# Kernel tuning notes

Measured on AMD Instinct MI355X. Metric: run time of the kernel, lower is better.

Reference implementation:

```python
import math
import jax, jax.numpy as jnp
import numpy as np

B, T, E = 2, 2048, 1024
H, KV = 16, 4
D = E // H          # 64
G = H // KV         # 4 groups


def rotate_half(x):
    x1, x2 = jnp.split(x, 2, axis=-1)
    return jnp.concatenate([-x2, x1], axis=-1)


def setup_inputs() -> dict:
    key = jax.random.key(0)
    ks = jax.random.split(key, 12)
    query = jax.random.normal(ks[0], (B, T, E), jnp.float32)
    key_t = jax.random.normal(ks[1], (B, T, E), jnp.float32)
    value = jax.random.normal(ks[2], (B, T, E), jnp.float32)
    # RoPE tables: [T, D]
    inv_freq = 1.0 / (10000.0 ** (np.arange(0, D, 2, dtype=np.float32) / D))
    pos = np.arange(T, dtype=np.float32)
    freqs = np.outer(pos, inv_freq)                      # [T, D/2]
    emb = np.concatenate([freqs, freqs], axis=-1)        # [T, D]
    cos_emb = jnp.asarray(np.cos(emb), jnp.float32)
    sin_emb = jnp.asarray(np.sin(emb), jnp.float32)
    # causal mask [1,1,T,T], True = keep
    mask = jnp.tril(jnp.ones((T, T), bool))[None, None, :, :]
    s = 0.02
    Wq = jax.random.normal(ks[3], (E, H * D), jnp.float32) * s
    bq = jnp.zeros((H * D,), jnp.float32)
    Wk = jax.random.normal(ks[4], (E, KV * D), jnp.float32) * s
    bk = jnp.zeros((KV * D,), jnp.float32)
    Wv = jax.random.normal(ks[5], (E, KV * D), jnp.float32) * s
    bv = jnp.zeros((KV * D,), jnp.float32)
    Wo = jax.random.normal(ks[6], (E, E), jnp.float32) * s
    bo = jnp.zeros((E,), jnp.float32)
    return {"query": query, "key": key_t, "value": value,
            "cos_emb": cos_emb, "sin_emb": sin_emb, "mask": mask,
            "Wq": Wq, "bq": bq, "Wk": Wk, "bk": bk,
            "Wv": Wv, "bv": bv, "Wo": Wo, "bo": bo}


def reference(query, key, value, cos_emb, sin_emb, mask,
              Wq, bq, Wk, bk, Wv, bv, Wo, bo):
    Bq, Tq, _ = query.shape
    Tk = key.shape[1]
    q = (query @ Wq + bq).reshape(Bq, Tq, H, D)          # [B,Tq,H,D]
    k = (key @ Wk + bk).reshape(Bq, Tk, KV, D)           # [B,Tk,KV,D]
    v = (value @ Wv + bv).reshape(Bq, Tk, KV, D)
    # expand kv heads across groups (head h = kv*G + g, consecutive repeat)
    k = jnp.repeat(k, G, axis=2)                         # [B,Tk,H,D]
    v = jnp.repeat(v, G, axis=2)
    # RoPE (applied post-expansion, as in the original)
    cos = cos_emb[None, :, None, :]                      # [1,T,1,D]
    sin = sin_emb[None, :, None, :]
    q = q * cos[:, :Tq] + rotate_half(q) * sin[:, :Tq]
    k = k * cos[:, :Tk] + rotate_half(k) * sin[:, :Tk]
    scores = jnp.einsum('bqhd,bkhd->bhqk', q, k) / math.sqrt(D)
    scores = jnp.where(mask[:, :, :Tq, :Tk], scores, jnp.float32(-jnp.inf))
    probs = jax.nn.softmax(scores, axis=-1)              # [B,H,Tq,Tk]
    attn = jnp.einsum('bhqk,bkhd->bqhd', probs, v).reshape(Bq, Tq, E)
    return attn @ Wo + bo
```

## Files before the change

### kernel.cpp

```cpp
#include <hip/hip_runtime.h>
#include <hip/hip_bf16.h>

constexpr int Bc  = 2;
constexpr int Tc  = 2048;
constexpr int Ec  = 1024;
constexpr int Hc  = 16;
constexpr int KVc = 4;
constexpr int Dc  = 64;

typedef short bf16x8 __attribute__((ext_vector_type(8)));
typedef short short4v __attribute__((ext_vector_type(4)));
typedef float f32x4  __attribute__((ext_vector_type(4)));
typedef float f32x16 __attribute__((ext_vector_type(16)));
typedef int   i32x4  __attribute__((ext_vector_type(4)));

__device__ inline short f2bf_bits(float f) {
    union { __hip_bfloat16 h; short s; } u;
    u.h = __float2bfloat16(f);
    return u.s;
}

__device__ inline float bf2f(short s) {
    union { short s16; __hip_bfloat16 h; } u;
    u.s16 = s;
    return __bfloat162float(u.h);
}

__device__ inline unsigned pkbf(float a, float b) {
    return (unsigned)(unsigned short)f2bf_bits(a)
         | ((unsigned)(unsigned short)f2bf_bits(b) << 16);
}

__device__ inline float fexp2(float x) { return __builtin_exp2f(x); }

__device__ inline void gload16(const short* g, short* lds) {
    __builtin_amdgcn_global_load_lds(
        (const __attribute__((address_space(1))) unsigned int*)g,
        (__attribute__((address_space(3))) unsigned int*)lds,
        16, 0, 0);
}

__global__ __launch_bounds__(256) void conv3_f32_bf16(
    const float* __restrict__ q, const float* __restrict__ k,
    const float* __restrict__ v,
    short* __restrict__ Xq, short* __restrict__ Xk, short* __restrict__ Xv)
{
    const int range = blockIdx.x >> 12;
    const int sub   = blockIdx.x & 4095;
    const float* x = range == 0 ? q : (range == 1 ? k : v);
    short*       y = range == 0 ? Xq : (range == 1 ? Xk : Xv);
    int i = (sub * 256 + threadIdx.x) * 4;
    float4 vv = *reinterpret_cast<const float4*>(x + i);
    short4v o;
    o[0] = f2bf_bits(vv.x);
    o[1] = f2bf_bits(vv.y);
    o[2] = f2bf_bits(vv.z);
    o[3] = f2bf_bits(vv.w);
    *reinterpret_cast<short4v*>(y + i) = o;
}

__global__ __launch_bounds__(256) void transp_all(
    const float* __restrict__ Wq, const float* __restrict__ Wk,
    const float* __restrict__ Wv, const float* __restrict__ Wo,
    short* __restrict__ Wqt, short* __restrict__ Wkt,
    short* __restrict__ Wvt, short* __restrict__ Wot)
{
    __shared__ float tile[32][33];
    const int id = blockIdx.x;
    const float* W; short* Wt; int N, bx, by;
    if (id < 1024)      { W = Wq; Wt = Wqt; N = 1024; bx = id & 31;          by = id >> 5; }
    else if (id < 1280) { W = Wk; Wt = Wkt; N = 256;  bx = (id - 1024) & 7;  by = (id - 1024) >> 3; }
    else if (id < 1536) { W = Wv; Wt = Wvt; N = 256;  bx = (id - 1280) & 7;  by = (id - 1280) >> 3; }
    else                { W = Wo; Wt = Wot; N = 1024; bx = (id - 1536) & 31; by = (id - 1536) >> 5; }
    const int K = 1024;
    int nb = bx * 32, kb = by * 32;
    int tx = threadIdx.x & 31, ty = threadIdx.x >> 5;
    #pragma unroll
    for (int j = 0; j < 4; ++j)
        tile[ty + j * 8][tx] = W[(size_t)(kb + ty + j * 8) * N + nb + tx];
    __syncthreads();
    #pragma unroll
    for (int j = 0; j < 4; ++j)
        Wt[(size_t)(nb + ty + j * 8) * K + kb + tx] = f2bf_bits(tile[tx][ty + j * 8]);
}

#define GEMM_CORE(A_, Bt_, Kdim_)                                              \
    const int lane = threadIdx.x & 63;                                         \
    const int w    = threadIdx.x >> 6;                                         \
    const int wm   = w >> 1, wn = w & 1;                                       \
    const int rin  = lane >> 3;                                                \
    const int swc  = ((lane & 7) ^ rin) * 8;                                   \
    f32x4 acc[4][2] = {};                                                      \
    for (int k0 = 0; k0 < (Kdim_); k0 += 64) {                                 \
        _Pragma("unroll")                                                      \
        for (int i2 = 0; i2 < 4; ++i2) {                                       \
            const int r = w * 32 + i2 * 8;                                     \
            gload16((A_) + (size_t)(m0 + r + rin) * (Kdim_) + k0 + swc,        \
                    As + r * 64);                                              \
        }                                                                      \
        _Pragma("unroll")                                                      \
        for (int i2 = 0; i2 < 2; ++i2) {                                       \
            const int r = w * 16 + i2 * 8;                                     \
            gload16((Bt_) + (size_t)(n0 + r + rin) * (Kdim_) + k0 + swc,       \
                    Bs + r * 64);                                              \
        }                                                                      \
        __syncthreads();                                                       \
        _Pragma("unroll")                                                      \
        for (int ks = 0; ks < 2; ++ks) {                                       \
            bf16x8 af[4], bfr[2];                                              \
            _Pragma("unroll")                                                  \
            for (int mi = 0; mi < 4; ++mi) {                                   \
                int row = wm * 64 + mi * 16 + (lane & 15);                     \
                int sl  = (ks * 4 + (lane >> 4)) ^ (row & 7);                  \
                af[mi] = *reinterpret_cast<const bf16x8*>(As + row * 64 + sl * 8); \
            }                                                                  \
            _Pragma("unroll")                                                  \
            for (int ni = 0; ni < 2; ++ni) {                                   \
                int row = wn * 32 + ni * 16 + (lane & 15);                     \
                int sl  = (ks * 4 + (lane >> 4)) ^ (row & 7);                  \
                bfr[ni] = *reinterpret_cast<const bf16x8*>(Bs + row * 64 + sl * 8); \
            }                                                                  \
            _Pragma("unroll")                                                  \
            for (int mi = 0; mi < 4; ++mi)                                     \
                _Pragma("unroll")                                              \
                for (int ni = 0; ni < 2; ++ni)                                 \
                    acc[mi][ni] = __builtin_amdgcn_mfma_f32_16x16x32_bf16(     \
                        af[mi], bfr[ni], acc[mi][ni], 0, 0, 0);                \
        }                                                                      \
        __syncthreads();                                                       \
    }

__global__ __launch_bounds__(256) void gemm_qkv(
    const short* __restrict__ Xq, const short* __restrict__ Xk,
    const short* __restrict__ Xv,
    const short* __restrict__ Wqt, const short* __restrict__ Wkt,
    const short* __restrict__ Wvt,
    const float* __restrict__ bq, const float* __restrict__ bk,
    const float* __restrict__ bv,
    short* __restrict__ Qp, short* __restrict__ Kp, short* __restrict__ VTp)
{
    __shared__ short As[128 * 64];
    __shared__ short Bs[64 * 64];
    const int gid = blockIdx.x;
    const short *A, *Bt; const float* bias; int bx, by, mode;
    if (gid < 512)      { mode = 0; A = Xq; Bt = Wqt; bias = bq; bx = gid & 15;         by = gid >> 4; }
    else if (gid < 640) { mode = 1; A = Xk; Bt = Wkt; bias = bk; bx = (gid - 512) & 3;  by = (gid - 512) >> 2; }
    else                { mode = 2; A = Xv; Bt = Wvt; bias = bv; bx = (gid - 640) & 3;  by = (gid - 640) >> 2; }
    const int m0 = by * 128, n0 = bx * 64;

    GEMM_CORE(A, Bt, 1024)

    #pragma unroll
    for (int mi = 0; mi < 4; ++mi)
        #pragma unroll
        for (int ni = 0; ni < 2; ++ni) {
            int col = n0 + wn * 32 + ni * 16 + (lane & 15);
            float bv2 = bias[col];
            #pragma unroll
            for (int i = 0; i < 4; ++i) {
                int row = m0 + wm * 64 + mi * 16 + ((lane >> 4) * 4) + i;
                float v = acc[mi][ni][i] + bv2;
                if (mode == 0)
                    Qp[(size_t)row * 1024 + col] = f2bf_bits(v);
                else if (mode == 1)
                    Kp[(size_t)row * 256 + col] = f2bf_bits(v);
                else
                    VTp[(((size_t)(row >> 11) * 256 + col) << 11) + (row & 2047)]
                        = f2bf_bits(v);
            }
        }
}

__global__ __launch_bounds__(256) void gemm_o(
    const short* __restrict__ A, const short* __restrict__ Bt,
    const float* __restrict__ bias, float* __restrict__ C)
{
    __shared__ short As[128 * 64];
    __shared__ short Bs[64 * 64];
    const int m0 = blockIdx.y * 128, n0 = blockIdx.x * 64;

    GEMM_CORE(A, Bt, 1024)

    #pragma unroll
    for (int mi = 0; mi < 4; ++mi)
        #pragma unroll
        for (int ni = 0; ni < 2; ++ni) {
            int col = n0 + wn * 32 + ni * 16 + (lane & 15);
            float bv2 = bias[col];
            #pragma unroll
            for (int i = 0; i < 4; ++i) {
                int row = m0 + wm * 64 + mi * 16 + ((lane >> 4) * 4) + i;
                C[(size_t)row * 1024 + col] = acc[mi][ni][i] + bv2;
            }
        }
}

__global__ __launch_bounds__(256) void rope_merged(
    short* __restrict__ Qp, short* __restrict__ Kp,
    const float* __restrict__ cosE, const float* __restrict__ sinE)
{
    short* x; int hbits; float scale; int idx;
    if (blockIdx.x < 2048) {
        x = Qp; hbits = 4; scale = 0.125f * 1.44269504089f;
        idx = blockIdx.x * 256 + threadIdx.x;
    } else {
        x = Kp; hbits = 2; scale = 1.0f;
        idx = (blockIdx.x - 2048) * 256 + threadIdx.x;
    }
    int dq  = (idx & 7) * 4;
    int hh  = (idx >> 3) & ((1 << hbits) - 1);
    int row = idx >> (3 + hbits);
    int t   = row & (Tc - 1);
    float4 c4 = *reinterpret_cast<const float4*>(cosE + t * 64 + dq);
    float4 s4 = *reinterpret_cast<const float4*>(sinE + t * 64 + dq);
    size_t base = (size_t)row * (64 << hbits) + hh * 64 + dq;
    short4v a = *reinterpret_cast<const short4v*>(x + base);
    short4v b = *reinterpret_cast<const short4v*>(x + base + 32);
    short4v oa, ob;
    float c[4] = {c4.x, c4.y, c4.z, c4.w};
    float s[4] = {s4.x, s4.y, s4.z, s4.w};
    #pragma unroll
    for (int j = 0; j < 4; ++j) {
        float x1 = bf2f(a[j]), x2 = bf2f(b[j]);
        oa[j] = f2bf_bits((x1 * c[j] - x2 * s[j]) * scale);
        ob[j] = f2bf_bits((x2 * c[j] + x1 * s[j]) * scale);
    }
    *reinterpret_cast<short4v*>(x + base)      = oa;
    *reinterpret_cast<short4v*>(x + base + 32) = ob;
}

__global__ __launch_bounds__(256, 4) void flash_gqa4(
    const short* __restrict__ Q,
    const short* __restrict__ Kx,
    const short* __restrict__ VT,
    short* __restrict__ attn,
    short* __restrict__ PO,
    float* __restrict__ ML)
{
    __shared__ short smem[16384];

    const int lane = threadIdx.x & 63;
    const int w    = threadIdx.x >> 6;
    const int lo   = lane & 31;
    const int hi   = lane >> 5;

    const int L   = blockIdx.x;
    const int xcd = L & 7;
    const int j   = L >> 3;
    const int g   = j & 3;
    const int u   = 39 - (j >> 2);
    int qt = 0, rem = u;
    while (true) { int nc0 = (qt >> 2) + 1; if (rem < nc0) break; rem -= nc0; ++qt; }
    const int c  = rem;
    const int nc = (qt >> 2) + 1;
    const int b   = xcd >> 2;
    const int kvh = xcd & 3;
    const int h   = kvh * 4 + g;
    const int slot = (b * 16 + h) * 40 + u;

    const int q0w = qt * 128 + w * 32;
    const int qg  = q0w + lo;

    bf16x8 qf[4];
    {
        const short* qp = Q + (size_t)(b * Tc + qg) * Ec + h * 64 + hi * 8;
        #pragma unroll
        for (int ds = 0; ds < 4; ++ds)
            qf[ds] = *reinterpret_cast<const bf16x8*>(qp + 16 * ds);
    }
    const short* Kb = Kx + (size_t)b * Tc * (KVc * Dc) + kvh * 64;
    const short* Vb = VT + (size_t)(b * KVc + kvh) * 64 * Tc;

    const int rin = lane >> 3;
    const int swc = ((lane & 7) ^ rin) * 8;
    auto stage = [&](int bufi, int kb2) {
        #pragma unroll
        for (int i2 = 0; i2 < 2; ++i2) {
            const int row = w * 16 + i2 * 8;
            gload16(Kb + (size_t)(kb2 + row + rin) * 256 + swc,
                    smem + bufi * 4096 + row * 64);
            gload16(Vb + (size_t)(row + rin) * Tc + kb2 + swc,
                    smem + 8192 + bufi * 4096 + row * 64);
        }
    };

    const int t0 = c * 8;
    const int t1 = min(c * 8 + 8, 2 * qt + 2);
    stage(0, t0 * 64);

    float m = -1e30f, l = 0.f;
    f32x16 o0 = {}, o1 = {};
    const int kv_hi = q0w + 32;

    for (int t = t0; t < t1; ++t) {
        const int kb  = t * 64;
        const int cur = (t - t0) & 1;
        if (t + 1 < t1) {
            stage(cur ^ 1, kb + 64);
            asm volatile("s_waitcnt vmcnt(4)" ::: "memory");
        } else {
            asm volatile("s_waitcnt vmcnt(0)" ::: "memory");
        }
        __builtin_amdgcn_s_barrier();

        if (kb < kv_hi) {
            const short* Kl = smem + cur * 4096;
            const short* Vl = smem + 8192 + cur * 4096;
            bf16x8 kf[2][4], vf[2][4];
            #pragma unroll
            for (int t2 = 0; t2 < 2; ++t2)
                #pragma unroll
                for (int ds = 0; ds < 4; ++ds) {
                    int row = 32 * t2 + lo;
                    int sl  = (2 * ds + hi) ^ (lo & 7);
                    kf[t2][ds] = *reinterpret_cast<const bf16x8*>(Kl + row * 64 + sl * 8);
                }
            #pragma unroll
            for (int td = 0; td < 2; ++td)
                #pragma unroll
                for (int sl2 = 0; sl2 < 4; ++sl2) {
                    int row = 32 * td + lo;
                    int sl  = (2 * sl2 + hi) ^ (lo & 7);
                    vf[td][sl2] = *reinterpret_cast<const bf16x8*>(Vl + row * 64 + sl * 8);
                }

            f32x16 s0 = {}, s1 = {};
            #pragma unroll
            for (int ds = 0; ds < 4; ++ds) {
                s0 = __builtin_amdgcn_mfma_f32_32x32x16_bf16(kf[0][ds], qf[ds], s0, 0, 0, 0);
                s1 = __builtin_amdgcn_mfma_f32_32x32x16_bf16(kf[1][ds], qf[ds], s1, 0, 0, 0);
            }

            if (kb + 63 > q0w) {
                #pragma unroll
                for (int r = 0; r < 16; ++r) {
                    int kkl = (r & 3) + 8 * (r >> 2) + 4 * hi;
                    if (kb + kkl > qg)      s0[r] = -1e30f;
                    if (kb + 32 + kkl > qg) s1[r] = -1e30f;
                }
            }

            float mx[8];
            #pragma unroll
            for (int j2 = 0; j2 < 8; ++j2)
                mx[j2] = fmaxf(fmaxf(s0[2 * j2], s0[2 * j2 + 1]),
                               fmaxf(s1[2 * j2], s1[2 * j2 + 1]));
            #pragma unroll
            for (int st = 4; st > 0; st >>= 1)
                #pragma unroll
                for (int j2 = 0; j2 < st; ++j2) mx[j2] = fmaxf(mx[j2], mx[j2 + st]);
            float pm = fmaxf(mx[0], __shfl_xor(mx[0], 32));

            float corr = 1.0f;
            if (__any(pm > m + 8.0f)) {
                float mn = fmaxf(m, pm);
                corr = fexp2(m - mn);
                m = mn;
                #pragma unroll
                for (int r = 0; r < 16; ++r) { o0[r] *= corr; o1[r] *= corr; }
            }
            float rs = 0.f;
            #pragma unroll
            for (int r = 0; r < 16; ++r) {
                s0[r] = fexp2(s0[r] - m);
                s1[r] = fexp2(s1[r] - m);
                rs += s0[r] + s1[r];
            }
            rs += __shfl_xor(rs, 32);
            l = l * corr + rs;

            #pragma unroll
            for (int t2 = 0; t2 < 2; ++t2) {
                f32x16 sv = t2 ? s1 : s0;
                unsigned wv[8], sx[8];
                #pragma unroll
                for (int j2 = 0; j2 < 8; ++j2) wv[j2] = pkbf(sv[2 * j2], sv[2 * j2 + 1]);
                #pragma unroll
                for (int j2 = 0; j2 < 8; ++j2) sx[j2] = __shfl_xor(wv[j2], 32);
                #pragma unroll
                for (int u2 = 0; u2 < 2; ++u2) {
                    union { unsigned u4[4]; bf16x8 v; } pf;
                    pf.u4[0] = hi ? sx[4 * u2 + 2] : wv[4 * u2];
                    pf.u4[1] = hi ? sx[4 * u2 + 3] : wv[4 * u2 + 1];
                    pf.u4[2] = hi ? wv[4 * u2 + 2] : sx[4 * u2];
                    pf.u4[3] = hi ? wv[4 * u2 + 3] : sx[4 * u2 + 1];
                    int sl = 2 * t2 + u2;
                    o0 = __builtin_amdgcn_mfma_f32_32x32x16_bf16(vf[0][sl], pf.v, o0, 0, 0, 0);
                    o1 = __builtin_amdgcn_mfma_f32_32x32x16_bf16(vf[1][sl], pf.v, o1, 0, 0, 0);
                }
            }
        }
        __builtin_amdgcn_s_barrier();
    }

    const float inv = (nc == 1) ? (1.0f / l) : 1.0f;
    short* ob = smem + w * 2048;
    #pragma unroll
    for (int r = 0; r < 16; ++r) {
        int d0 = (r & 3) + 8 * (r >> 2) + 4 * hi;
        ob[lo * 64 + ( d0       ^ ((lo & 7) << 3))] = f2bf_bits(o0[r] * inv);
        ob[lo * 64 + ((d0 + 32) ^ ((lo & 7) << 3))] = f2bf_bits(o1[r] * inv);
    }
    if (nc > 1 && hi == 0) {
        ML[(size_t)slot * 256 + (w * 32 + lo) * 2]     = m;
        ML[(size_t)slot * 256 + (w * 32 + lo) * 2 + 1] = l;
    }
    #pragma unroll
    for (int j2 = 0; j2 < 4; ++j2) {
        int row = lane >> 1;
        int c8  = ((lane & 1) * 4 + j2) * 8;
        bf16x8 v = *reinterpret_cast<const bf16x8*>(
            ob + row * 64 + (c8 ^ ((row & 7) << 3)));
        if (nc == 1)
            *reinterpret_cast<bf16x8*>(
                attn + (size_t)(b * Tc + q0w + row) * Ec + h * 64 + c8) = v;
        else
            *reinterpret_cast<bf16x8*>(
                PO + (size_t)slot * 8192 + (w * 32 + row) * 64 + c8) = v;
    }
}

__global__ __launch_bounds__(256) void combine_kernel(
    const short* __restrict__ PO, const float* __restrict__ ML,
    short* __restrict__ attn)
{
    const int qt    = 4 + (blockIdx.x >> 2);
    const int rg    = blockIdx.x & 3;
    const int combo = blockIdx.y;
    const int h = combo & 15, b = combo >> 4;
    const int nc = (qt >> 2) + 1;
    const int k  = qt >> 2, r4 = qt & 3;
    const int base = (k + 1) * (2 * k + r4);
    const int slot0 = combo * 40 + base;

    const int r  = rg * 32 + (threadIdx.x >> 3);
    const int d8 = (threadIdx.x & 7) * 8;

    float mv[4], lv[4];
    float M = -1e30f;
    #pragma unroll 4
    for (int cc = 0; cc < nc; ++cc) {
        mv[cc] = ML[(size_t)(slot0 + cc) * 256 + r * 2];
        lv[cc] = ML[(size_t)(slot0 + cc) * 256 + r * 2 + 1];
        M = fmaxf(M, mv[cc]);
    }
    float Lsum = 0.f;
    float a[8] = {};
    #pragma unroll 4
    for (int cc = 0; cc < nc; ++cc) {
        float wgt = fexp2(mv[cc] - M);
        Lsum += wgt * lv[cc];
        bf16x8 po = *reinterpret_cast<const bf16x8*>(
            PO + (size_t)(slot0 + cc) * 8192 + r * 64 + d8);
        #pragma unroll
        for (int j = 0; j < 8; ++j) a[j] += wgt * bf2f(po[j]);
    }
    float inv = 1.0f / Lsum;
    bf16x8 o;
    #pragma unroll
    for (int j = 0; j < 8; ++j) o[j] = f2bf_bits(a[j] * inv);
    *reinterpret_cast<bf16x8*>(
        attn + (size_t)(b * Tc + qt * 128 + r) * Ec + h * 64 + d8) = o;
}

extern "C" void kernel_launch(void* const* d_in, const int* in_sizes, int n_in,
                              void* d_out, int out_size, void* d_ws, size_t ws_size,
                              hipStream_t stream)
{
    const float* query = (const float*)d_in[0];
    const float* key   = (const float*)d_in[1];
    const float* value = (const float*)d_in[2];
    const float* cosE  = (const float*)d_in[3];
    const float* sinE  = (const float*)d_in[4];
    const float* Wq = (const float*)d_in[6];
    const float* bq = (const float*)d_in[7];
    const float* Wk = (const float*)d_in[8];
    const float* bk = (const float*)d_in[9];
    const float* Wv = (const float*)d_in[10];
    const float* bv = (const float*)d_in[11];
    const float* Wo = (const float*)d_in[12];
    const float* bo = (const float*)d_in[13];

    char* ws = (char*)d_ws;
    constexpr size_t MB = 1u << 20;
    short* Xq   = (short*)(ws + 0);
    short* Xk   = (short*)(ws + 8  * MB);
    short* Xv   = (short*)(ws + 16 * MB);
    short* Wqt  = (short*)(ws + 24 * MB);
    short* Wkt  = (short*)(ws + 26 * MB);
    short* Wvt  = (short*)(ws + 26 * MB + 512 * 1024);
    short* Wot  = (short*)(ws + 27 * MB);
    short* Qp   = (short*)(ws + 29 * MB);
    short* Kp   = (short*)(ws + 37 * MB);
    short* VTp  = (short*)(ws + 39 * MB);
    short* attn = (short*)(ws + 41 * MB);
    short* PO   = (short*)(ws + 0);
    float* ML   = (float*)(ws + 21 * MB);
    (void)ws_size;

    conv3_f32_bf16<<<12288, 256, 0, stream>>>(query, key, value, Xq, Xk, Xv);
    transp_all<<<2560, 256, 0, stream>>>(Wq, Wk, Wv, Wo, Wqt, Wkt, Wvt, Wot);
    gemm_qkv<<<768, 256, 0, stream>>>(Xq, Xk, Xv, Wqt, Wkt, Wvt,
                                      bq, bk, bv, Qp, Kp, VTp);
    rope_merged<<<2560, 256, 0, stream>>>(Qp, Kp, cosE, sinE);
    flash_gqa4<<<1280, 256, 0, stream>>>(Qp, Kp, VTp, attn, PO, ML);
    combine_kernel<<<dim3(48, 32), 256, 0, stream>>>(PO, ML, attn);
    gemm_o<<<dim3(16, 32), 256, 0, stream>>>(attn, Wot, bo, (float*)d_out);
}
```

Before: 134.5 us.

## Enlarge GEMM tiles to 128x128, reorder flash K/V loads, use packed bf16 convert

The QKV and output-projection GEMMs move from 128x64 to 128x128 block tiles, halving the block count so each B tile is reused across more rows of A. The flash kernel now loads K fragments per half and issues QK MFMAs before loading V fragments, aiming to shorten register live ranges. It also drops the 4-blocks-per-CU launch bound. bf16 packing switches to a paired conversion intrinsic. Larger tiles add accumulator registers and LDS per block and launch fewer blocks (256 for gemm_o), which may underfill the GPU.

```diff
diff --git a/kernel.cpp b/kernel.cpp
--- a/kernel.cpp
+++ b/kernel.cpp
@@ -27,8 +27,9 @@
 }
 
 __device__ inline unsigned pkbf(float a, float b) {
-    return (unsigned)(unsigned short)f2bf_bits(a)
-         | ((unsigned)(unsigned short)f2bf_bits(b) << 16);
+    union { __hip_bfloat162 h2; unsigned u; } u;
+    u.h2 = __float22bfloat162_rn(float2{a, b});
+    return u.u;
 }
 
 __device__ inline float fexp2(float x) { return __builtin_exp2f(x); }
@@ -84,30 +85,26 @@
         Wt[(size_t)(nb + ty + j * 8) * K + kb + tx] = f2bf_bits(tile[tx][ty + j * 8]);
 }
 
-#define GEMM_CORE(A_, Bt_, Kdim_)                                              \
+#define GEMM_CORE128(A_, Bt_, Kdim_)                                           \
     const int lane = threadIdx.x & 63;                                         \
     const int w    = threadIdx.x >> 6;                                         \
     const int wm   = w >> 1, wn = w & 1;                                       \
     const int rin  = lane >> 3;                                                \
     const int swc  = ((lane & 7) ^ rin) * 8;                                   \
-    f32x4 acc[4][2] = {};                                                      \
+    f32x4 acc[4][4] = {};                                                      \
     for (int k0 = 0; k0 < (Kdim_); k0 += 64) {                                 \
         _Pragma("unroll")                                                      \
         for (int i2 = 0; i2 < 4; ++i2) {                                       \
             const int r = w * 32 + i2 * 8;                                     \
             gload16((A_) + (size_t)(m0 + r + rin) * (Kdim_) + k0 + swc,        \
                     As + r * 64);                                              \
-        }                                                                      \
-        _Pragma("unroll")                                                      \
-        for (int i2 = 0; i2 < 2; ++i2) {                                       \
-            const int r = w * 16 + i2 * 8;                                     \
             gload16((Bt_) + (size_t)(n0 + r + rin) * (Kdim_) + k0 + swc,       \
                     Bs + r * 64);                                              \
         }                                                                      \
         __syncthreads();                                                       \
         _Pragma("unroll")                                                      \
         for (int ks = 0; ks < 2; ++ks) {                                       \
-            bf16x8 af[4], bfr[2];                                              \
+            bf16x8 af[4], bfr[4];                                              \
             _Pragma("unroll")                                                  \
             for (int mi = 0; mi < 4; ++mi) {                                   \
                 int row = wm * 64 + mi * 16 + (lane & 15);                     \
@@ -115,15 +112,15 @@
                 af[mi] = *reinterpret_cast<const bf16x8*>(As + row * 64 + sl * 8); \
             }                                                                  \
             _Pragma("unroll")                                                  \
-            for (int ni = 0; ni < 2; ++ni) {                                   \
-                int row = wn * 32 + ni * 16 + (lane & 15);                     \
+            for (int ni = 0; ni < 4; ++ni) {                                   \
+                int row = wn * 64 + ni * 16 + (lane & 15);                     \
                 int sl  = (ks * 4 + (lane >> 4)) ^ (row & 7);                  \
                 bfr[ni] = *reinterpret_cast<const bf16x8*>(Bs + row * 64 + sl * 8); \
             }                                                                  \
             _Pragma("unroll")                                                  \
             for (int mi = 0; mi < 4; ++mi)                                     \
                 _Pragma("unroll")                                              \
-                for (int ni = 0; ni < 2; ++ni)                                 \
+                for (int ni = 0; ni < 4; ++ni)                                 \
                     acc[mi][ni] = __builtin_amdgcn_mfma_f32_16x16x32_bf16(     \
                         af[mi], bfr[ni], acc[mi][ni], 0, 0, 0);                \
         }                                                                      \
@@ -140,21 +137,21 @@
     short* __restrict__ Qp, short* __restrict__ Kp, short* __restrict__ VTp)
 {
     __shared__ short As[128 * 64];
-    __shared__ short Bs[64 * 64];
+    __shared__ short Bs[128 * 64];
     const int gid = blockIdx.x;
     const short *A, *Bt; const float* bias; int bx, by, mode;
-    if (gid < 512)      { mode = 0; A = Xq; Bt = Wqt; bias = bq; bx = gid & 15;         by = gid >> 4; }
-    else if (gid < 640) { mode = 1; A = Xk; Bt = Wkt; bias = bk; bx = (gid - 512) & 3;  by = (gid - 512) >> 2; }
-    else                { mode = 2; A = Xv; Bt = Wvt; bias = bv; bx = (gid - 640) & 3;  by = (gid - 640) >> 2; }
-    const int m0 = by * 128, n0 = bx * 64;
-
-    GEMM_CORE(A, Bt, 1024)
+    if (gid < 256)      { mode = 0; A = Xq; Bt = Wqt; bias = bq; bx = gid & 7;         by = gid >> 3; }
+    else if (gid < 320) { mode = 1; A = Xk; Bt = Wkt; bias = bk; bx = (gid - 256) & 1; by = (gid - 256) >> 1; }
+    else                { mode = 2; A = Xv; Bt = Wvt; bias = bv; bx = (gid - 320) & 1; by = (gid - 320) >> 1; }
+    const int m0 = by * 128, n0 = bx * 128;
+
+    GEMM_CORE128(A, Bt, 1024)
 
     #pragma unroll
     for (int mi = 0; mi < 4; ++mi)
         #pragma unroll
-        for (int ni = 0; ni < 2; ++ni) {
-            int col = n0 + wn * 32 + ni * 16 + (lane & 15);
+        for (int ni = 0; ni < 4; ++ni) {
+            int col = n0 + wn * 64 + ni * 16 + (lane & 15);
             float bv2 = bias[col];
             #pragma unroll
             for (int i = 0; i < 4; ++i) {
@@ -176,16 +173,16 @@
     const float* __restrict__ bias, float* __restrict__ C)
 {
     __shared__ short As[128 * 64];
-    __shared__ short Bs[64 * 64];
-    const int m0 = blockIdx.y * 128, n0 = blockIdx.x * 64;
-
-    GEMM_CORE(A, Bt, 1024)
+    __shared__ short Bs[128 * 64];
+    const int m0 = blockIdx.y * 128, n0 = blockIdx.x * 128;
+
+    GEMM_CORE128(A, Bt, 1024)
 
     #pragma unroll
     for (int mi = 0; mi < 4; ++mi)
         #pragma unroll
-        for (int ni = 0; ni < 2; ++ni) {
-            int col = n0 + wn * 32 + ni * 16 + (lane & 15);
+        for (int ni = 0; ni < 4; ++ni) {
+            int col = n0 + wn * 64 + ni * 16 + (lane & 15);
             float bv2 = bias[col];
             #pragma unroll
             for (int i = 0; i < 4; ++i) {
@@ -229,7 +226,7 @@
     *reinterpret_cast<short4v*>(x + base + 32) = ob;
 }
 
-__global__ __launch_bounds__(256, 4) void flash_gqa4(
+__global__ __launch_bounds__(256) void flash_gqa5(
     const short* __restrict__ Q,
     const short* __restrict__ Kx,
     const short* __restrict__ VT,
@@ -306,15 +303,67 @@
         if (kb < kv_hi) {
             const short* Kl = smem + cur * 4096;
             const short* Vl = smem + 8192 + cur * 4096;
-            bf16x8 kf[2][4], vf[2][4];
-            #pragma unroll
-            for (int t2 = 0; t2 < 2; ++t2)
+
+            f32x16 s0 = {}, s1 = {};
+            #pragma unroll
+            for (int t2 = 0; t2 < 2; ++t2) {
+                bf16x8 kf[4];
                 #pragma unroll
                 for (int ds = 0; ds < 4; ++ds) {
                     int row = 32 * t2 + lo;
                     int sl  = (2 * ds + hi) ^ (lo & 7);
-                    kf[t2][ds] = *reinterpret_cast<const bf16x8*>(Kl + row * 64 + sl * 8);
+                    kf[ds] = *reinterpret_cast<const bf16x8*>(Kl + row * 64 + sl * 8);
                 }
+                if (t2 == 0) {
+                    #pragma unroll
+                    for (int ds = 0; ds < 4; ++ds)
+                        s0 = __builtin_amdgcn_mfma_f32_32x32x16_bf16(kf[ds], qf[ds], s0, 0, 0, 0);
+                } else {
+                    #pragma unroll
+                    for (int ds = 0; ds < 4; ++ds)
+                        s1 = __builtin_amdgcn_mfma_f32_32x32x16_bf16(kf[ds], qf[ds], s1, 0, 0, 0);
+                }
+            }
+
+            if (kb + 63 > q0w) {
+                #pragma unroll
+                for (int r = 0; r < 16; ++r) {
+                    int kkl = (r & 3) + 8 * (r >> 2) + 4 * hi;
+                    if (kb + kkl > qg)      s0[r] = -1e30f;
+                    if (kb + 32 + kkl > qg) s1[r] = -1e30f;
+                }
+            }
+
+            float mx[8];
+            #pragma unroll
+            for (int j2 = 0; j2 < 8; ++j2)
+                mx[j2] = fmaxf(fmaxf(s0[2 * j2], s0[2 * j2 + 1]),
+                               fmaxf(s1[2 * j2], s1[2 * j2 + 1]));
+            #pragma unroll
+            for (int st = 4; st > 0; st >>= 1)
+                #pragma unroll
+                for (int j2 = 0; j2 < st; ++j2) mx[j2] = fmaxf(mx[j2], mx[j2 + st]);
+            float pm = fmaxf(mx[0], __shfl_xor(mx[0], 32));
+
+            float corr = 1.0f;
+            if (__any(pm > m + 8.0f)) {
+                float mn = fmaxf(m, pm);
+                corr = fexp2(m - mn);
+                m = mn;
+                #pragma unroll
+                for (int r = 0; r < 16; ++r) { o0[r] *= corr; o1[r] *= corr; }
+            }
+            float rs = 0.f;
+            #pragma unroll
+            for (int r = 0; r < 16; ++r) {
+                s0[r] = fexp2(s0[r] - m);
+                s1[r] = fexp2(s1[r] - m);
+                rs += s0[r] + s1[r];
+            }
+            rs += __shfl_xor(rs, 32);
+            l = l * corr + rs;
+
+            bf16x8 vf[2][4];
             #pragma unroll
             for (int td = 0; td < 2; ++td)
                 #pragma unroll
@@ -323,51 +372,6 @@
                     int sl  = (2 * sl2 + hi) ^ (lo & 7);
                     vf[td][sl2] = *reinterpret_cast<const bf16x8*>(Vl + row * 64 + sl * 8);
                 }
-
-            f32x16 s0 = {}, s1 = {};
-            #pragma unroll
-            for (int ds = 0; ds < 4; ++ds) {
-                s0 = __builtin_amdgcn_mfma_f32_32x32x16_bf16(kf[0][ds], qf[ds], s0, 0, 0, 0);
-                s1 = __builtin_amdgcn_mfma_f32_32x32x16_bf16(kf[1][ds], qf[ds], s1, 0, 0, 0);
-            }
-
-            if (kb + 63 > q0w) {
-                #pragma unroll
-                for (int r = 0; r < 16; ++r) {
-                    int kkl = (r & 3) + 8 * (r >> 2) + 4 * hi;
-                    if (kb + kkl > qg)      s0[r] = -1e30f;
-                    if (kb + 32 + kkl > qg) s1[r] = -1e30f;
-                }
-            }
-
-            float mx[8];
-            #pragma unroll
-            for (int j2 = 0; j2 < 8; ++j2)
-                mx[j2] = fmaxf(fmaxf(s0[2 * j2], s0[2 * j2 + 1]),
-                               fmaxf(s1[2 * j2], s1[2 * j2 + 1]));
-            #pragma unroll
-            for (int st = 4; st > 0; st >>= 1)
-                #pragma unroll
-                for (int j2 = 0; j2 < st; ++j2) mx[j2] = fmaxf(mx[j2], mx[j2 + st]);
-            float pm = fmaxf(mx[0], __shfl_xor(mx[0], 32));
-
-            float corr = 1.0f;
-            if (__any(pm > m + 8.0f)) {
-                float mn = fmaxf(m, pm);
-                corr = fexp2(m - mn);
-                m = mn;
-                #pragma unroll
-                for (int r = 0; r < 16; ++r) { o0[r] *= corr; o1[r] *= corr; }
-            }
-            float rs = 0.f;
-            #pragma unroll
-            for (int r = 0; r < 16; ++r) {
-                s0[r] = fexp2(s0[r] - m);
-                s1[r] = fexp2(s1[r] - m);
-                rs += s0[r] + s1[r];
-            }
-            rs += __shfl_xor(rs, 32);
-            l = l * corr + rs;
 
             #pragma unroll
             for (int t2 = 0; t2 < 2; ++t2) {
@@ -500,10 +504,10 @@
 
     conv3_f32_bf16<<<12288, 256, 0, stream>>>(query, key, value, Xq, Xk, Xv);
     transp_all<<<2560, 256, 0, stream>>>(Wq, Wk, Wv, Wo, Wqt, Wkt, Wvt, Wot);
-    gemm_qkv<<<768, 256, 0, stream>>>(Xq, Xk, Xv, Wqt, Wkt, Wvt,
+    gemm_qkv<<<384, 256, 0, stream>>>(Xq, Xk, Xv, Wqt, Wkt, Wvt,
                                       bq, bk, bv, Qp, Kp, VTp);
     rope_merged<<<2560, 256, 0, stream>>>(Qp, Kp, cosE, sinE);
-    flash_gqa4<<<1280, 256, 0, stream>>>(Qp, Kp, VTp, attn, PO, ML);
+    flash_gqa5<<<1280, 256, 0, stream>>>(Qp, Kp, VTp, attn, PO, ML);
     combine_kernel<<<dim3(48, 32), 256, 0, stream>>>(PO, ML, attn);
-    gemm_o<<<dim3(16, 32), 256, 0, stream>>>(attn, Wot, bo, (float*)d_out);
-}
+    gemm_o<<<dim3(8, 32), 256, 0, stream>>>(attn, Wot, bo, (float*)d_out);
+}
```

Result: slower. 141.2 us (+5.0%).
